# Performance work log

Measured on AMD Instinct MI355X. Metric: run time of the kernel, lower is better.

Reference implementation:

```python
import jax, jax.numpy as jnp
import numpy as np

E4M3_MAX = 448.0


def fp8_qdq(x):
    """Per-tensor fp8 (e4m3) quantize-dequantize with amax scaling."""
    amax = jnp.max(jnp.abs(x))
    scale = jnp.maximum(amax / E4M3_MAX, 1e-12).astype(x.dtype)
    q = (x / scale).astype(jnp.float8_e4m3fn).astype(x.dtype)
    return q * scale


def setup_inputs() -> dict:
    key = jax.random.key(0)
    k1, k2, k3 = jax.random.split(key, 3)
    A, B, C, D, E = 4, 512, 512, 32, 128
    inputs = jax.random.normal(k1, (A, B, C), dtype=jnp.float32)
    kernel1 = jax.random.normal(k2, (C, D, E), dtype=jnp.float32) * 0.02
    kernel2 = jax.random.normal(k3, (C, D, E), dtype=jnp.float32) * 0.02
    return {"inputs": inputs, "kernel1": kernel1, "kernel2": kernel2}


def reference(inputs, kernel1, kernel2):
    # Layer 1: EinsumDenseFp8('abc,cde->abde')
    x_q = fp8_qdq(inputs)
    w1_q = fp8_qdq(kernel1)
    h = jnp.einsum('abc,cde->abde', x_q, w1_q)  # (A,B,D,E)
    # Layer 2: EinsumDenseFp8('abde,cde->abce', is_last=True)
    h_q = fp8_qdq(h)
    w2_q = fp8_qdq(kernel2)
    out = jnp.einsum('abde,cde->abce', h_q, w2_q)  # (A,B,C,E)
    return out
```

## Files before the change

### kernel.cpp

```cpp
#include <hip/hip_runtime.h>

typedef float f32x4 __attribute__((ext_vector_type(4)));

#define AX_X 0
#define AX_W1 1
#define AX_W2 2

__device__ __forceinline__ unsigned char fp8_encode(float t) {
  unsigned tb = __float_as_uint(t);
  unsigned sgn = (tb >> 24) & 0x80u;
  float a = fabsf(t);
  unsigned sb = (unsigned)(int)rintf(a * 512.0f);
  unsigned u = tb & 0x7fffffffu;
  unsigned rem = u & 0xFFFFFu;
  unsigned keep = u & ~0xFFFFFu;
  unsigned inc = (rem > 0x80000u || (rem == 0x80000u && (keep & 0x100000u))) ? 0x100000u : 0u;
  keep += inc;
  int e = (int)(keep >> 23) - 127;
  unsigned nb = (unsigned)((e + 7) << 3) | ((keep >> 20) & 7u);
  unsigned b = (a < 0.015625f) ? sb : nb;
  return (unsigned char)(b | sgn);
}

__device__ __forceinline__ float scale_from(const float* __restrict__ part, int which) {
  float m = 0.f;
#pragma unroll
  for (int i = 0; i < 64; i++) m = fmaxf(m, part[which * 64 + i]);
  return fmaxf(m / 448.0f, 1e-12f);
}

__device__ __forceinline__ float scale_raw(float rawmax) {
  return fmaxf(rawmax / 448.0f, 1e-12f);
}

__global__ __launch_bounds__(256, 4) void k_amax3(const float* __restrict__ x,
                                                  const float* __restrict__ w1,
                                                  const float* __restrict__ w2,
                                                  float* __restrict__ part) {
  __shared__ float wmax[4];
  int which = blockIdx.y;
  const float* p = which == 0 ? x : (which == 1 ? w1 : w2);
  int n4 = which == 0 ? (1048576 / 4) : (2097152 / 4);
  float m = 0.f;
  for (int i = blockIdx.x * 256 + threadIdx.x; i < n4; i += gridDim.x * 256) {
    float4 v = ((const float4*)p)[i];
    m = fmaxf(m, fmaxf(fmaxf(fabsf(v.x), fabsf(v.y)), fmaxf(fabsf(v.z), fabsf(v.w))));
  }
  for (int off = 32; off; off >>= 1) m = fmaxf(m, __shfl_xor(m, off));
  int t = threadIdx.x;
  if ((t & 63) == 0) wmax[t >> 6] = m;
  __syncthreads();
  if (t == 0)
    part[which * 64 + blockIdx.x] =
        fmaxf(fmaxf(wmax[0], wmax[1]), fmaxf(wmax[2], wmax[3]));
}

__global__ __launch_bounds__(256, 2) void k_quant_all(const float* __restrict__ x,
                                                      const float* __restrict__ w1,
                                                      const float* __restrict__ w2,
                                                      unsigned char* __restrict__ qx,
                                                      unsigned char* __restrict__ qw1t,
                                                      unsigned char* __restrict__ qw2,
                                                      const float* __restrict__ part) {
  __shared__ float tile[64 * 68];
  int b = blockIdx.x, t = threadIdx.x;
  if (b < 256) {
    float s = scale_from(part, AX_X);
    int i = b * 256 + t;
    const float4* src = (const float4*)x + (size_t)i * 4;
    union { unsigned char bb[16]; uint4 u; } o;
#pragma unroll
    for (int p = 0; p < 4; p++) {
      float4 v = src[p];
      o.bb[p * 4 + 0] = fp8_encode(v.x / s);
      o.bb[p * 4 + 1] = fp8_encode(v.y / s);
      o.bb[p * 4 + 2] = fp8_encode(v.z / s);
      o.bb[p * 4 + 3] = fp8_encode(v.w / s);
    }
    *(uint4*)(qx + (size_t)i * 16) = o.u;
  } else if (b < 768) {
    float s = scale_from(part, AX_W1);
    int idx = b - 256;
    int n0 = (idx & 63) * 64, c0 = (idx >> 6) * 64;
    int row = t >> 2, q4 = t & 3;
    const float* src = w1 + (size_t)(c0 + row) * 4096 + n0 + q4 * 16;
#pragma unroll
    for (int p = 0; p < 4; p++) {
      float4 v = *(const float4*)(src + p * 4);
      *(float4*)&tile[row * 68 + q4 * 16 + p * 4] = v;
    }
    __syncthreads();
    int nl = t >> 2, ch = t & 3;
    union { unsigned char bb[16]; uint4 u; } o;
#pragma unroll
    for (int j = 0; j < 16; j++) o.bb[j] = fp8_encode(tile[(ch * 16 + j) * 68 + nl] / s);
    *(uint4*)(qw1t + (size_t)(n0 + nl) * 512 + c0 + ch * 16) = o.u;
  } else {
    float s = scale_from(part, AX_W2);
    int row = b - 768;
    const float* sp = w2 + (size_t)row * 4096;
#pragma unroll
    for (int p = 0; p < 4; p++) {
      int n = (p * 256 + t) * 4;
      float4 v = *(const float4*)(sp + n);
      *(float4*)&tile[(n >> 7) * 132 + (n & 127)] = v;
    }
    __syncthreads();
    int e = t >> 1, half = t & 1;
    union { unsigned char bb[16]; uint4 u; } o;
#pragma unroll
    for (int j = 0; j < 16; j++) o.bb[j] = fp8_encode(tile[(half * 16 + j) * 132 + e] / s);
    *(uint4*)(qw2 + ((size_t)e * 512 + row) * 32 + half * 16) = o.u;
  }
}

__global__ __launch_bounds__(256, 2) void k_quant_h(const float* __restrict__ src,
                                                    unsigned char* __restrict__ dst,
                                                    const float* __restrict__ hpart) {
  __shared__ float tile[32 * 132];
  int row = blockIdx.x, t = threadIdx.x;
  float2 hv = ((const float2*)hpart)[t];
  float m = fmaxf(hv.x, hv.y);
  for (int off = 32; off; off >>= 1) m = fmaxf(m, __shfl_xor(m, off));
  if ((t & 63) == 0) tile[t >> 6] = m;
  __syncthreads();
  float s = scale_raw(fmaxf(fmaxf(tile[0], tile[1]), fmaxf(tile[2], tile[3])));
  __syncthreads();
  const float* sp = src + (size_t)row * 4096;
#pragma unroll
  for (int p = 0; p < 4; p++) {
    int n = (p * 256 + t) * 4;
    float4 v = *(const float4*)(sp + n);
    *(float4*)&tile[(n >> 7) * 132 + (n & 127)] = v;
  }
  __syncthreads();
  int e = t >> 1, half = t & 1;
  union { unsigned char b[16]; uint4 u; } o;
#pragma unroll
  for (int j = 0; j < 16; j++) o.b[j] = fp8_encode(tile[(half * 16 + j) * 132 + e] / s);
  *(uint4*)(dst + ((size_t)e * 2048 + row) * 32 + half * 16) = o.u;
}

__global__ __launch_bounds__(256, 3) void k_gemm1(const unsigned char* __restrict__ qa,
                                                  const unsigned char* __restrict__ qb,
                                                  float* __restrict__ h,
                                                  const float* __restrict__ part,
                                                  float* __restrict__ hpart) {
  __shared__ float wred[4];
  int m0 = blockIdx.y * 128, n0 = blockIdx.x * 128;
  int t = threadIdx.x, lane = t & 63, w = t >> 6, wr = w >> 1, wc = w & 1;
  f32x4 acc[4][4] = {};
  const int ko = (lane >> 4) << 3;
  const unsigned char* ap = qa + (size_t)(m0 + wr * 64 + (lane & 15)) * 512 + ko;
  const unsigned char* bp = qb + (size_t)(n0 + wc * 64 + (lane & 15)) * 512 + ko;

  for (int k0 = 0; k0 < 512; k0 += 32) {
    long a[4], b[4];
#pragma unroll
    for (int i = 0; i < 4; i++) {
      a[i] = *(const long*)(ap + (size_t)i * 16 * 512 + k0);
      b[i] = *(const long*)(bp + (size_t)i * 16 * 512 + k0);
    }
#pragma unroll
    for (int mi = 0; mi < 4; mi++)
#pragma unroll
      for (int ni = 0; ni < 4; ni++)
        acc[mi][ni] = __builtin_amdgcn_mfma_f32_16x16x32_fp8_fp8(a[mi], b[ni], acc[mi][ni], 0, 0, 0);
  }

  float s1 = scale_from(part, AX_X) * scale_from(part, AX_W1);
  float lmax = 0.f;
#pragma unroll
  for (int mi = 0; mi < 4; mi++)
#pragma unroll
    for (int ni = 0; ni < 4; ni++)
#pragma unroll
      for (int r = 0; r < 4; r++) {
        float v = acc[mi][ni][r] * s1;
        h[(size_t)(m0 + wr * 64 + mi * 16 + ((lane >> 4) << 2) + r) * 4096 +
          (n0 + wc * 64 + ni * 16 + (lane & 15))] = v;
        lmax = fmaxf(lmax, fabsf(v));
      }
  for (int off = 32; off; off >>= 1) lmax = fmaxf(lmax, __shfl_xor(lmax, off));
  if (lane == 0) wred[w] = lmax;
  __syncthreads();
  if (t == 0)
    hpart[blockIdx.y * 32 + blockIdx.x] =
        fmaxf(fmaxf(wred[0], wred[1]), fmaxf(wred[2], wred[3]));
}

__global__ __launch_bounds__(512, 2) void k_gemm2(const unsigned char* __restrict__ qh,
                                                  const unsigned char* __restrict__ qw2,
                                                  const float* __restrict__ part,
                                                  const float* __restrict__ hpart,
                                                  float* __restrict__ out) {
  __shared__ float lbuf[8 * 64 * 34];
  int bid = blockIdx.x;
  int sw = (bid & 7) * 256 + (bid >> 3);
  int m0 = (sw >> 5) * 32, c0 = (sw & 31) * 16;
  int t = threadIdx.x, lane = t & 63, w = t >> 6;
  float m = hpart[t];
  for (int off = 32; off; off >>= 1) m = fmaxf(m, __shfl_xor(m, off));
  if (lane == 0) lbuf[w] = m;
  __syncthreads();
  float hm = lbuf[0];
#pragma unroll
  for (int i = 1; i < 8; i++) hm = fmaxf(hm, lbuf[i]);
  float s2 = scale_raw(hm) * scale_from(part, AX_W2);
  __syncthreads();

  int mw = m0 + (w >> 2) * 16;
  int e0 = (w & 3) * 32;
  const unsigned char* A = qh + ((size_t)e0 * 2048 + mw + (lane & 15)) * 32 + ((lane >> 4) << 3);
  const unsigned char* B = qw2 + ((size_t)e0 * 512 + c0 + (lane & 15)) * 32 + ((lane >> 4) << 3);
  f32x4 acc[32];
#pragma unroll
  for (int e = 0; e < 32; e++) {
    long a = *(const long*)(A + (size_t)e * 2048 * 32);
    long b = *(const long*)(B + (size_t)e * 512 * 32);
    f32x4 z = {0.f, 0.f, 0.f, 0.f};
    acc[e] = __builtin_amdgcn_mfma_f32_16x16x32_fp8_fp8(a, b, z, 0, 0, 0);
  }
  float* lw = lbuf + w * (64 * 34);
#pragma unroll
  for (int r = 0; r < 4; r++) {
#pragma unroll
    for (int g = 0; g < 8; g++) {
      *(float2*)&lw[lane * 34 + 4 * g] =
          make_float2(acc[4 * g + 0][r] * s2, acc[4 * g + 1][r] * s2);
      *(float2*)&lw[lane * 34 + 4 * g + 2] =
          make_float2(acc[4 * g + 2][r] * s2, acc[4 * g + 3][r] * s2);
    }
#pragma unroll
    for (int i = 0; i < 8; i++) {
      int p = i * 8 + (lane >> 3);
      float2 u0 = *(const float2*)&lw[p * 34 + (lane & 7) * 4];
      float2 u1 = *(const float2*)&lw[p * 34 + (lane & 7) * 4 + 2];
      float* dst = out + ((size_t)(mw + ((p >> 4) << 2) + r) * 512 + c0 + (p & 15)) * 128 +
                   e0 + (lane & 7) * 4;
      f32x4 vv = {u0.x, u0.y, u1.x, u1.y};
      __builtin_nontemporal_store(vv, (f32x4*)dst);
    }
  }
}

extern "C" void kernel_launch(void* const* d_in, const int* in_sizes, int n_in,
                              void* d_out, int out_size, void* d_ws, size_t ws_size,
                              hipStream_t stream) {
  const float* x  = (const float*)d_in[0];
  const float* w1 = (const float*)d_in[1];
  const float* w2 = (const float*)d_in[2];
  float* out = (float*)d_out;

  float* part  = (float*)d_ws;
  float* hpart = (float*)d_ws + 256;
  unsigned char* base = (unsigned char*)d_ws + 4096;
  unsigned char* qx   = base;
  unsigned char* qw1t = qx   + (size_t)2048 * 512;
  unsigned char* qw2  = qw1t + (size_t)4096 * 512;
  unsigned char* qh   = qw2  + (size_t)128 * 512 * 32;
  float* h = (float*)(qh + (size_t)128 * 2048 * 32);

  k_amax3<<<dim3(64, 3), dim3(256), 0, stream>>>(x, w1, w2, part);
  k_quant_all<<<dim3(1280), dim3(256), 0, stream>>>(x, w1, w2, qx, qw1t, qw2, part);
  k_gemm1<<<dim3(32, 16), dim3(256), 0, stream>>>(qx, qw1t, h, part, hpart);
  k_quant_h<<<dim3(2048), dim3(256), 0, stream>>>(h, qh, hpart);
  k_gemm2<<<dim3(2048), dim3(512), 0, stream>>>(qh, qw2, part, hpart, out);
}
```

Baseline: 181.6 us.

## Retile gemm1 to 64x64 with LDS staging and coalesced epilogue stores

gemm1 now uses 64x64 tiles, so the grid goes from 512 to 2048 blocks. Each k-step stages the A and B tiles into LDS via global_load_lds, replacing direct per-lane global loads. The epilogue goes through an LDS buffer so h is written with coalesced nontemporal float4 stores. The hpart partial-max count grows to 2048, so quant_h and gemm2 now reduce it with vectorized loads. There is no double buffering and each k-step needs two barriers, so load latency is exposed and partly relies on higher occupancy to hide it.

```diff
diff --git a/kernel.cpp b/kernel.cpp
--- a/kernel.cpp
+++ b/kernel.cpp
@@ -33,6 +33,12 @@
   return fmaxf(rawmax / 448.0f, 1e-12f);
 }
 
+__device__ __forceinline__ void gll16(const void* g, void* l) {
+  __builtin_amdgcn_global_load_lds(
+      (const __attribute__((address_space(1))) unsigned int*)g,
+      (__attribute__((address_space(3))) unsigned int*)l, 16, 0, 0);
+}
+
 __global__ __launch_bounds__(256, 4) void k_amax3(const float* __restrict__ x,
                                                   const float* __restrict__ w1,
                                                   const float* __restrict__ w2,
@@ -119,8 +125,10 @@
                                                     const float* __restrict__ hpart) {
   __shared__ float tile[32 * 132];
   int row = blockIdx.x, t = threadIdx.x;
-  float2 hv = ((const float2*)hpart)[t];
-  float m = fmaxf(hv.x, hv.y);
+  float4 a4 = ((const float4*)hpart)[t * 2];
+  float4 b4 = ((const float4*)hpart)[t * 2 + 1];
+  float m = fmaxf(fmaxf(fmaxf(a4.x, a4.y), fmaxf(a4.z, a4.w)),
+                  fmaxf(fmaxf(b4.x, b4.y), fmaxf(b4.z, b4.w)));
   for (int off = 32; off; off >>= 1) m = fmaxf(m, __shfl_xor(m, off));
   if ((t & 63) == 0) tile[t >> 6] = m;
   __syncthreads();
@@ -141,51 +149,66 @@
   *(uint4*)(dst + ((size_t)e * 2048 + row) * 32 + half * 16) = o.u;
 }
 
-__global__ __launch_bounds__(256, 3) void k_gemm1(const unsigned char* __restrict__ qa,
+__global__ __launch_bounds__(256, 4) void k_gemm1(const unsigned char* __restrict__ qa,
                                                   const unsigned char* __restrict__ qb,
                                                   float* __restrict__ h,
                                                   const float* __restrict__ part,
                                                   float* __restrict__ hpart) {
+  __shared__ unsigned char As[2048], Bs[2048];
+  __shared__ float ebuf[4 * 32 * 36];
   __shared__ float wred[4];
-  int m0 = blockIdx.y * 128, n0 = blockIdx.x * 128;
+  int m0 = blockIdx.y * 64, n0 = blockIdx.x * 64;
   int t = threadIdx.x, lane = t & 63, w = t >> 6, wr = w >> 1, wc = w & 1;
-  f32x4 acc[4][4] = {};
-  const int ko = (lane >> 4) << 3;
-  const unsigned char* ap = qa + (size_t)(m0 + wr * 64 + (lane & 15)) * 512 + ko;
-  const unsigned char* bp = qb + (size_t)(n0 + wc * 64 + (lane & 15)) * 512 + ko;
+  f32x4 acc[2][2] = {};
+  const unsigned char* sg = (t < 128)
+      ? qa + (size_t)(m0 + (t >> 1)) * 512 + (t & 1) * 16
+      : qb + (size_t)(n0 + ((t - 128) >> 1)) * 512 + (t & 1) * 16;
+  unsigned char* sdst = (t < 128) ? As + t * 16 : Bs + (t - 128) * 16;
+  const int abase = (wr * 32 + (lane & 15)) * 32 + ((lane >> 4) << 3);
+  const int bbase = (wc * 32 + (lane & 15)) * 32 + ((lane >> 4) << 3);
 
   for (int k0 = 0; k0 < 512; k0 += 32) {
-    long a[4], b[4];
-#pragma unroll
-    for (int i = 0; i < 4; i++) {
-      a[i] = *(const long*)(ap + (size_t)i * 16 * 512 + k0);
-      b[i] = *(const long*)(bp + (size_t)i * 16 * 512 + k0);
-    }
-#pragma unroll
-    for (int mi = 0; mi < 4; mi++)
-#pragma unroll
-      for (int ni = 0; ni < 4; ni++)
+    gll16(sg + k0, sdst);
+    __syncthreads();
+    long a[2], b[2];
+    a[0] = *(const long*)(As + abase);
+    a[1] = *(const long*)(As + abase + 16 * 32);
+    b[0] = *(const long*)(Bs + bbase);
+    b[1] = *(const long*)(Bs + bbase + 16 * 32);
+#pragma unroll
+    for (int mi = 0; mi < 2; mi++)
+#pragma unroll
+      for (int ni = 0; ni < 2; ni++)
         acc[mi][ni] = __builtin_amdgcn_mfma_f32_16x16x32_fp8_fp8(a[mi], b[ni], acc[mi][ni], 0, 0, 0);
+    __syncthreads();
   }
 
   float s1 = scale_from(part, AX_X) * scale_from(part, AX_W1);
   float lmax = 0.f;
-#pragma unroll
-  for (int mi = 0; mi < 4; mi++)
-#pragma unroll
-    for (int ni = 0; ni < 4; ni++)
+  float* ew = ebuf + w * (32 * 36);
+#pragma unroll
+  for (int mi = 0; mi < 2; mi++)
+#pragma unroll
+    for (int ni = 0; ni < 2; ni++)
 #pragma unroll
       for (int r = 0; r < 4; r++) {
         float v = acc[mi][ni][r] * s1;
-        h[(size_t)(m0 + wr * 64 + mi * 16 + ((lane >> 4) << 2) + r) * 4096 +
-          (n0 + wc * 64 + ni * 16 + (lane & 15))] = v;
+        ew[(mi * 16 + ((lane >> 4) << 2) + r) * 36 + ni * 16 + (lane & 15)] = v;
         lmax = fmaxf(lmax, fabsf(v));
       }
+#pragma unroll
+  for (int p = 0; p < 4; p++) {
+    int row = p * 8 + (lane >> 3);
+    float4 u = *(const float4*)&ew[row * 36 + (lane & 7) * 4];
+    float* dst = h + (size_t)(m0 + wr * 32 + row) * 4096 + n0 + wc * 32 + (lane & 7) * 4;
+    f32x4 vv = {u.x, u.y, u.z, u.w};
+    __builtin_nontemporal_store(vv, (f32x4*)dst);
+  }
   for (int off = 32; off; off >>= 1) lmax = fmaxf(lmax, __shfl_xor(lmax, off));
   if (lane == 0) wred[w] = lmax;
   __syncthreads();
   if (t == 0)
-    hpart[blockIdx.y * 32 + blockIdx.x] =
+    hpart[blockIdx.y * 64 + blockIdx.x] =
         fmaxf(fmaxf(wred[0], wred[1]), fmaxf(wred[2], wred[3]));
 }
 
@@ -199,7 +222,8 @@
   int sw = (bid & 7) * 256 + (bid >> 3);
   int m0 = (sw >> 5) * 32, c0 = (sw & 31) * 16;
   int t = threadIdx.x, lane = t & 63, w = t >> 6;
-  float m = hpart[t];
+  float4 a4 = ((const float4*)hpart)[t];
+  float m = fmaxf(fmaxf(a4.x, a4.y), fmaxf(a4.z, a4.w));
   for (int off = 32; off; off >>= 1) m = fmaxf(m, __shfl_xor(m, off));
   if (lane == 0) lbuf[w] = m;
   __syncthreads();
@@ -254,7 +278,7 @@
 
   float* part  = (float*)d_ws;
   float* hpart = (float*)d_ws + 256;
-  unsigned char* base = (unsigned char*)d_ws + 4096;
+  unsigned char* base = (unsigned char*)d_ws + 16384;
   unsigned char* qx   = base;
   unsigned char* qw1t = qx   + (size_t)2048 * 512;
   unsigned char* qw2  = qw1t + (size_t)4096 * 512;
@@ -263,7 +287,7 @@
 
   k_amax3<<<dim3(64, 3), dim3(256), 0, stream>>>(x, w1, w2, part);
   k_quant_all<<<dim3(1280), dim3(256), 0, stream>>>(x, w1, w2, qx, qw1t, qw2, part);
-  k_gemm1<<<dim3(32, 16), dim3(256), 0, stream>>>(qx, qw1t, h, part, hpart);
+  k_gemm1<<<dim3(64, 32), dim3(256), 0, stream>>>(qx, qw1t, h, part, hpart);
   k_quant_h<<<dim3(2048), dim3(256), 0, stream>>>(h, qh, hpart);
   k_gemm2<<<dim3(2048), dim3(512), 0, stream>>>(qh, qw2, part, hpart, out);
 }
```

New measurement: 170.6 us. 1.06x faster.
